# Kernel tuning notes

Hardware: AMD Instinct MI355X
Metric: run time of the kernel (lower is better)

Reference implementation:

```python
import jax, jax.numpy as jnp
import numpy as np

N = 2048      # num_nodes
B = 16        # batch
D_IN = 2      # input_dim per node
UNITS = 64    # rnn_units
F = D_IN + UNITS   # concat feature size = 66
M = 3         # num_matrices = (1 support + 1 adp hop)*K(=1) + 1 identity
E = N * 16    # sparse support edges (avg degree 16)


def _spmm(rows, cols, vals, x):
    # sparse support @ x, x: (N, K); equivalent of torch.sparse.mm
    return jax.ops.segment_sum(vals[:, None] * x[cols], rows, num_segments=N)


def _gconv(inputs, state, W, support_rows, support_cols, support_vals, adp):
    # inputs: (B, N*D_IN), state: (B, N*units) -> out: (B, N*out_dim)
    x = jnp.concatenate([inputs.reshape(B, N, -1), state.reshape(B, N, -1)], axis=2)  # (B,N,F)
    f = x.shape[2]
    x0 = x.transpose(1, 2, 0).reshape(N, f * B)                # (N, F*B)
    # diffusion step 1 over the single random_walk support
    x1 = _spmm(support_rows, support_cols, support_vals, x0)   # (N, F*B)
    # adaptive adjacency, k_hop=1 -> adp_lst = [adp], applied to x0
    x_temp = x0.reshape(N, f, B).transpose(2, 0, 1)            # (B,N,F)
    x2 = jnp.einsum('bnm,bmf->bnf', adp, x_temp)               # (B,N,F)
    x2 = x2.transpose(1, 2, 0).reshape(N, f * B)
    xs = jnp.stack([x0, x1, x2], axis=0)                       # (M,N,F*B)
    xs = xs.reshape(M, N, f, B).transpose(3, 1, 2, 0).reshape(B * N, f * M)
    out = xs @ W                                               # (B*N, out_dim)  (no bias: source never adds it)
    return out.reshape(B, N * W.shape[1])


def setup_inputs() -> dict:
    key = jax.random.key(0)
    ks = jax.random.split(key, 8)
    inputs = jax.random.normal(ks[0], (B, N * D_IN), dtype=jnp.float32)
    hx = jax.random.normal(ks[1], (B, N * UNITS), dtype=jnp.float32)
    adp = jax.random.uniform(ks[2], (B, N, N), dtype=jnp.float32) / N  # ~row-stochastic adaptive adj
    support_rows = jax.random.randint(ks[3], (E,), 0, N, dtype=jnp.int32)
    support_cols = jax.random.randint(ks[4], (E,), 0, N, dtype=jnp.int32)
    support_vals = jax.random.uniform(ks[5], (E,), dtype=jnp.float32) / 16.0
    W_ru = jax.random.normal(ks[6], (F * M, 2 * UNITS), dtype=jnp.float32) * 0.05
    W_c = jax.random.normal(ks[7], (F * M, UNITS), dtype=jnp.float32) * 0.05
    return dict(inputs=inputs, hx=hx, adp=adp, support_rows=support_rows,
                support_cols=support_cols, support_vals=support_vals,
                W_ru=W_ru, W_c=W_c, time_axis=0)


def reference(inputs, hx, adp, support_rows, support_cols, support_vals, W_ru, W_c, time_axis):
    # GRU with graph convolution gates (use_gc_for_ru=True, activation=tanh)
    ru = jax.nn.sigmoid(_gconv(inputs, hx, W_ru, support_rows, support_cols, support_vals, adp))
    ru = ru.reshape(B, N, 2 * UNITS)
    r = ru[..., :UNITS].reshape(B, N * UNITS)
    u = ru[..., UNITS:].reshape(B, N * UNITS)
    c = jnp.tanh(_gconv(inputs, r * hx, W_c, support_rows, support_cols, support_vals, adp))
    return u * hx + (1.0 - u) * c
```

## Files before the change

### kernel.cpp

```cpp
#include <hip/hip_runtime.h>
#include <cstdint>
#include <cstddef>

#define DN 2048
#define DB 16
#define DE 32768
#define FPAD 96

typedef __bf16 bf16x8 __attribute__((ext_vector_type(8)));
typedef float f32x4 __attribute__((ext_vector_type(4)));

__global__ __launch_bounds__(256) void prep_kernel(
    const float* __restrict__ inputs, const float* __restrict__ hx,
    const float* __restrict__ Wru, const float* __restrict__ Wc,
    __bf16* __restrict__ xcat1, __bf16* __restrict__ xcat2,
    __bf16* __restrict__ wtru, __bf16* __restrict__ wtc) {
  int idx = blockIdx.x * 256 + threadIdx.x;
  const int T1 = DB * DN * FPAD;
  if (idx < 2 * T1) {
    int which = idx >= T1 ? 1 : 0;
    int i = idx - which * T1;
    int f = i % FPAD;
    int bn = i / FPAD;
    int n = bn & (DN - 1);
    int b = bn >> 11;
    __bf16 v = (__bf16)0.0f;
    if (f < 2) v = (__bf16)inputs[(b << 12) + n * 2 + f];
    else if (f < 66 && !which) v = (__bf16)hx[((size_t)b << 17) + (n << 6) + (f - 2)];
    if (which) xcat2[i] = v; else xcat1[i] = v;
  } else {
    int j = idx - 2 * T1;
    if (j < 384 * FPAD) {
      int k = j % FPAD, o = j / FPAD;
      wtru[j] = (k < 66) ? (__bf16)Wru[(k * 3 + (o >> 7)) * 128 + (o & 127)] : (__bf16)0.0f;
    } else {
      j -= 384 * FPAD;
      if (j < 192 * FPAD) {
        int k = j % FPAD, o = j / FPAD;
        wtc[j] = (k < 66) ? (__bf16)Wc[(k * 3 + (o >> 6)) * 64 + (o & 63)] : (__bf16)0.0f;
      }
    }
  }
}

__global__ __launch_bounds__(1024) void build_csr(
    const int* __restrict__ rows, const int* __restrict__ cols,
    const float* __restrict__ vals,
    int* __restrict__ csr_ptr, int* __restrict__ csr_col,
    float* __restrict__ csr_val) {
  __shared__ int cnt[DN];
  __shared__ int sa[DN];
  __shared__ int sb[DN];
  int t = threadIdx.x;
  cnt[t] = 0; cnt[t + 1024] = 0;
  __syncthreads();
  for (int e = t; e < DE; e += 1024) atomicAdd(&cnt[rows[e]], 1);
  __syncthreads();
  sa[t] = cnt[t]; sa[t + 1024] = cnt[t + 1024];
  __syncthreads();
  int* src = sa; int* dst = sb;
  for (int off = 1; off < DN; off <<= 1) {
    for (int i = t; i < DN; i += 1024) {
      int v = src[i];
      if (i >= off) v += src[i - off];
      dst[i] = v;
    }
    __syncthreads();
    int* tmp = src; src = dst; dst = tmp;
  }
  int e0 = src[t] - cnt[t];
  int e1 = src[t + 1024] - cnt[t + 1024];
  csr_ptr[t] = e0; csr_ptr[t + 1024] = e1;
  if (t == 0) csr_ptr[DN] = DE;
  dst[t] = e0; dst[t + 1024] = e1;
  __syncthreads();
  for (int e = t; e < DE; e += 1024) {
    int r = rows[e];
    int p = atomicAdd(&dst[r], 1);
    csr_col[p] = cols[e];
    csr_val[p] = vals[e];
  }
}

template <int OD>
__global__ __launch_bounds__(256) void small_gemm(
    const __bf16* __restrict__ A, const __bf16* __restrict__ Bt,
    float* __restrict__ Y0, __bf16* __restrict__ y1b, __bf16* __restrict__ y2b) {
  __shared__ __attribute__((aligned(16))) __bf16 As[128 * 104];
  __shared__ __attribute__((aligned(16))) __bf16 Bs[64 * 104];
  int tid = threadIdx.x;
  int wave = tid >> 6, lane = tid & 63;
  int lrow = lane & 15, quad = lane >> 4;
  int r0 = blockIdx.x * 128;
  int c0 = blockIdx.y * 64;
  const uint4* gA = (const uint4*)(A + (size_t)r0 * FPAD);
  const uint4* gB = (const uint4*)(Bt + (size_t)c0 * FPAD);
  uint4* sA = (uint4*)As;
  uint4* sB = (uint4*)Bs;
#pragma unroll
  for (int i = 0; i < 6; ++i) {
    int s = i * 256 + tid;
    int r = s / 12, c4 = s % 12;
    sA[r * 13 + c4] = gA[r * 12 + c4];
  }
#pragma unroll
  for (int i = 0; i < 3; ++i) {
    int s = i * 256 + tid;
    int r = s / 12, c4 = s % 12;
    sB[r * 13 + c4] = gB[r * 12 + c4];
  }
  __syncthreads();
  int wm = wave >> 1, wn = wave & 1;
  f32x4 acc[4][2];
#pragma unroll
  for (int mt = 0; mt < 4; ++mt)
#pragma unroll
    for (int nt = 0; nt < 2; ++nt) acc[mt][nt] = (f32x4){0.f, 0.f, 0.f, 0.f};
#pragma unroll
  for (int kk = 0; kk < 3; ++kk) {
    bf16x8 af[4], bv[2];
#pragma unroll
    for (int mt = 0; mt < 4; ++mt)
      af[mt] = *(const bf16x8*)(As + (wm * 64 + mt * 16 + lrow) * 104 + kk * 32 + quad * 8);
#pragma unroll
    for (int nt = 0; nt < 2; ++nt)
      bv[nt] = *(const bf16x8*)(Bs + (wn * 32 + nt * 16 + lrow) * 104 + kk * 32 + quad * 8);
#pragma unroll
    for (int mt = 0; mt < 4; ++mt)
#pragma unroll
      for (int nt = 0; nt < 2; ++nt)
        acc[mt][nt] = __builtin_amdgcn_mfma_f32_16x16x32_bf16(af[mt], bv[nt], acc[mt][nt], 0, 0, 0);
  }
#pragma unroll
  for (int mt = 0; mt < 4; ++mt)
#pragma unroll
    for (int nt = 0; nt < 2; ++nt)
#pragma unroll
      for (int r = 0; r < 4; ++r) {
        int row = r0 + wm * 64 + mt * 16 + quad * 4 + r;
        int col = c0 + wn * 32 + nt * 16 + lrow;
        float v = acc[mt][nt][r];
        int g = col >> ((OD == 128) ? 7 : 6);
        int oo = col & (OD - 1);
        size_t oi = (size_t)row * OD + oo;
        if (g == 0) Y0[oi] = v;
        else if (g == 1) y1b[oi] = (__bf16)v;
        else y2b[oi] = (__bf16)v;
      }
}

template <int OD>
__global__ __launch_bounds__(256) void gather_pre(
    float* __restrict__ Y0, const __bf16* __restrict__ y1b,
    const int* __restrict__ csr_ptr, const int* __restrict__ csr_col,
    const float* __restrict__ csr_val) {
  constexpr int SH = (OD == 128) ? 7 : 6;
  int idx = blockIdx.x * 256 + threadIdx.x;
  int o = idx & (OD - 1);
  int bn = idx >> SH;
  int n = bn & (DN - 1);
  int b = bn >> 11;
  float acc = Y0[idx];
  int e1 = csr_ptr[n + 1];
  const __bf16* yb = y1b + ((size_t)b << 11) * OD;
  for (int e = csr_ptr[n]; e < e1; ++e)
    acc += csr_val[e] * (float)yb[(size_t)csr_col[e] * OD + o];
  Y0[idx] = acc;
}

template <int OD>
__global__ void transpose_y2(const __bf16* __restrict__ y2b, __bf16* __restrict__ y2t) {
  __shared__ __bf16 tile[32][33];
  int b = blockIdx.z;
  int mb = blockIdx.x * 32, ob = blockIdx.y * 32;
  int tx = threadIdx.x, ty = threadIdx.y;
#pragma unroll
  for (int i = 0; i < 4; ++i)
    tile[ty + i * 8][tx] = y2b[(size_t)(b * DN + mb + ty + i * 8) * OD + ob + tx];
  __syncthreads();
#pragma unroll
  for (int i = 0; i < 4; ++i)
    y2t[(size_t)(b * OD + ob + ty + i * 8) * DN + mb + tx] = tile[tx][ty + i * 8];
}

template <int OD, int WGM, int WGN, int MT, int NT, bool IS_RU>
__global__ __launch_bounds__(256) void adp_gemm(
    const float* __restrict__ adp, const __bf16* __restrict__ y2t,
    const float* __restrict__ pre, const float* __restrict__ hx,
    float* __restrict__ u_buf, __bf16* __restrict__ xcat2,
    float* __restrict__ outp) {
  constexpr int BM = WGM * MT * 16;
  constexpr int BN = WGN * NT * 16;
  constexpr int LDK = 72;
  constexpr int NA = (BM * 8) / 256;
  constexpr int NB = (BN * 8) / 256;
  __shared__ __attribute__((aligned(16))) __bf16 As[BM * LDK];
  __shared__ __attribute__((aligned(16))) __bf16 Bs[BN * LDK];
  int tid = threadIdx.x;
  int wave = tid >> 6, lane = tid & 63;
  int lrow = lane & 15, quad = lane >> 4;
  int b = blockIdx.y;
  int row0 = blockIdx.x * BM;
  const float* Ab = adp + ((size_t)b * DN + row0) * DN;
  const __bf16* Bb = y2t + (size_t)b * OD * DN;
  int wm = wave / WGN, wn = wave % WGN;
  f32x4 acc[MT][NT];
#pragma unroll
  for (int mt = 0; mt < MT; ++mt)
#pragma unroll
    for (int nt = 0; nt < NT; ++nt) acc[mt][nt] = (f32x4){0.f, 0.f, 0.f, 0.f};

  for (int c = 0; c < DN / 64; ++c) {
    int k0 = c * 64;
    f32x4 ra[NA][2];
    uint4 rb[NB];
#pragma unroll
    for (int i = 0; i < NA; ++i) {
      int s = i * 256 + tid, r = s >> 3, cc = s & 7;
      const float* p = Ab + (size_t)r * DN + k0 + cc * 8;
      ra[i][0] = *(const f32x4*)p;
      ra[i][1] = *(const f32x4*)(p + 4);
    }
#pragma unroll
    for (int i = 0; i < NB; ++i) {
      int s = i * 256 + tid, r = s >> 3, cc = s & 7;
      rb[i] = *(const uint4*)(Bb + (size_t)r * DN + k0 + cc * 8);
    }
    __syncthreads();
#pragma unroll
    for (int i = 0; i < NA; ++i) {
      int s = i * 256 + tid, r = s >> 3, cc = s & 7;
      bf16x8 cv;
#pragma unroll
      for (int j = 0; j < 4; ++j) cv[j] = (__bf16)ra[i][0][j];
#pragma unroll
      for (int j = 0; j < 4; ++j) cv[4 + j] = (__bf16)ra[i][1][j];
      *(bf16x8*)(As + r * LDK + cc * 8) = cv;
    }
#pragma unroll
    for (int i = 0; i < NB; ++i) {
      int s = i * 256 + tid, r = s >> 3, cc = s & 7;
      *(uint4*)(Bs + r * LDK + cc * 8) = rb[i];
    }
    __syncthreads();
#pragma unroll
    for (int kk = 0; kk < 2; ++kk) {
      bf16x8 af[MT], bv[NT];
#pragma unroll
      for (int mt = 0; mt < MT; ++mt) {
        int r = wm * MT * 16 + mt * 16 + lrow;
        af[mt] = *(const bf16x8*)(As + r * LDK + (kk * 4 + quad) * 8);
      }
#pragma unroll
      for (int nt = 0; nt < NT; ++nt) {
        int r = wn * NT * 16 + nt * 16 + lrow;
        bv[nt] = *(const bf16x8*)(Bs + r * LDK + (kk * 4 + quad) * 8);
      }
#pragma unroll
      for (int mt = 0; mt < MT; ++mt)
#pragma unroll
        for (int nt = 0; nt < NT; ++nt)
          acc[mt][nt] = __builtin_amdgcn_mfma_f32_16x16x32_bf16(af[mt], bv[nt], acc[mt][nt], 0, 0, 0);
    }
  }
#pragma unroll
  for (int mt = 0; mt < MT; ++mt)
#pragma unroll
    for (int nt = 0; nt < NT; ++nt)
#pragma unroll
      for (int r = 0; r < 4; ++r) {
        int n = row0 + wm * MT * 16 + mt * 16 + quad * 4 + r;
        int o = wn * NT * 16 + nt * 16 + lrow;
        float g = acc[mt][nt][r] + pre[((size_t)b * DN + n) * OD + o];
        if (IS_RU) {
          float s = 1.f / (1.f + __expf(-g));
          if (o < 64) {
            float hxv = hx[((size_t)b << 17) + n * 64 + o];
            xcat2[((size_t)b * DN + n) * FPAD + 2 + o] = (__bf16)(s * hxv);
          } else {
            u_buf[((size_t)b * DN + n) * 64 + (o - 64)] = s;
          }
        } else {
          float cval = 1.f - 2.f / (__expf(2.f * g) + 1.f);
          float u = u_buf[((size_t)b * DN + n) * 64 + o];
          float hxv = hx[((size_t)b << 17) + n * 64 + o];
          outp[((size_t)b << 17) + n * 64 + o] = u * hxv + (1.f - u) * cval;
        }
      }
}

extern "C" void kernel_launch(void* const* d_in, const int* in_sizes, int n_in,
                              void* d_out, int out_size, void* d_ws, size_t ws_size,
                              hipStream_t stream) {
  const float* inputs = (const float*)d_in[0];
  const float* hx     = (const float*)d_in[1];
  const float* adp    = (const float*)d_in[2];
  const int* srows    = (const int*)d_in[3];
  const int* scols    = (const int*)d_in[4];
  const float* svals  = (const float*)d_in[5];
  const float* Wru    = (const float*)d_in[6];
  const float* Wc     = (const float*)d_in[7];
  float* outp = (float*)d_out;

  char* w = (char*)d_ws;
  auto carve = [&](size_t bytes) -> char* {
    char* p = w;
    w += (bytes + 255) & ~(size_t)255;
    return p;
  };
  int*    csr_ptr = (int*)   carve((DN + 1) * sizeof(int));
  int*    csr_col = (int*)   carve(DE * sizeof(int));
  float*  csr_val = (float*) carve(DE * sizeof(float));
  __bf16* xcat1   = (__bf16*)carve((size_t)DB * DN * FPAD * 2);
  __bf16* xcat2   = (__bf16*)carve((size_t)DB * DN * FPAD * 2);
  __bf16* wtru    = (__bf16*)carve(384 * FPAD * 2);
  __bf16* wtc     = (__bf16*)carve(192 * FPAD * 2);
  float*  Y0      = (float*) carve((size_t)DB * DN * 128 * 4);
  __bf16* y1b     = (__bf16*)carve((size_t)DB * DN * 128 * 2);
  __bf16* y2b     = (__bf16*)carve((size_t)DB * DN * 128 * 2);
  __bf16* y2t     = (__bf16*)carve((size_t)DB * DN * 128 * 2);
  float*  u_buf   = (float*) carve((size_t)DB * DN * 64 * 4);
  (void)ws_size; (void)in_sizes; (void)n_in; (void)out_size;

  prep_kernel<<<24792, 256, 0, stream>>>(inputs, hx, Wru, Wc, xcat1, xcat2, wtru, wtc);
  build_csr<<<1, 1024, 0, stream>>>(srows, scols, svals, csr_ptr, csr_col, csr_val);

  small_gemm<128><<<dim3(256, 6), 256, 0, stream>>>(xcat1, wtru, Y0, y1b, y2b);
  gather_pre<128><<<16384, 256, 0, stream>>>(Y0, y1b, csr_ptr, csr_col, csr_val);
  transpose_y2<128><<<dim3(64, 4, 16), dim3(32, 8), 0, stream>>>(y2b, y2t);
  adp_gemm<128, 2, 2, 4, 4, true><<<dim3(16, 16), 256, 0, stream>>>(
      adp, y2t, Y0, hx, u_buf, xcat2, outp);

  small_gemm<64><<<dim3(256, 3), 256, 0, stream>>>(xcat2, wtc, Y0, y1b, y2b);
  gather_pre<64><<<8192, 256, 0, stream>>>(Y0, y1b, csr_ptr, csr_col, csr_val);
  transpose_y2<64><<<dim3(64, 2, 16), dim3(32, 8), 0, stream>>>(y2b, y2t);
  adp_gemm<64, 4, 1, 2, 4, false><<<dim3(16, 16), 256, 0, stream>>>(
      adp, y2t, Y0, hx, u_buf, xcat2, outp);
}
```

Baseline: 804.0 us.

## Prefetch adp tiles into registers, shrink adp GEMM row tile, parallelize CSR build

The adp GEMM now loads the next K-chunk of adp and y2t into registers while MFMAs run on the current shared-memory tile, overlapping global loads with compute. The row tile drops from 128 to 64, which doubles the grid to 512 blocks for better occupancy across CUs. The single-block CSR build is split into multi-block count, scan and scatter kernels, with the counter zeroed inside prep_kernel. This adds more kernel launches and more register pressure from the prefetch buffers, and the smaller row tile makes each block reload the full y2t operand.

```diff
diff --git a/kernel.cpp b/kernel.cpp
--- a/kernel.cpp
+++ b/kernel.cpp
@@ -14,7 +14,8 @@
     const float* __restrict__ inputs, const float* __restrict__ hx,
     const float* __restrict__ Wru, const float* __restrict__ Wc,
     __bf16* __restrict__ xcat1, __bf16* __restrict__ xcat2,
-    __bf16* __restrict__ wtru, __bf16* __restrict__ wtc) {
+    __bf16* __restrict__ wtru, __bf16* __restrict__ wtc,
+    int* __restrict__ cnt) {
   int idx = blockIdx.x * 256 + threadIdx.x;
   const int T1 = DB * DN * FPAD;
   if (idx < 2 * T1) {
@@ -38,48 +39,55 @@
       if (j < 192 * FPAD) {
         int k = j % FPAD, o = j / FPAD;
         wtc[j] = (k < 66) ? (__bf16)Wc[(k * 3 + (o >> 6)) * 64 + (o & 63)] : (__bf16)0.0f;
-      }
-    }
-  }
-}
-
-__global__ __launch_bounds__(1024) void build_csr(
-    const int* __restrict__ rows, const int* __restrict__ cols,
-    const float* __restrict__ vals,
-    int* __restrict__ csr_ptr, int* __restrict__ csr_col,
-    float* __restrict__ csr_val) {
-  __shared__ int cnt[DN];
+      } else {
+        j -= 192 * FPAD;
+        if (j < DN) cnt[j] = 0;
+      }
+    }
+  }
+}
+
+__global__ __launch_bounds__(512) void csr_count(const int* __restrict__ rows,
+                                                 int* __restrict__ cnt) {
+  int e = blockIdx.x * 512 + threadIdx.x;
+  atomicAdd(&cnt[rows[e]], 1);
+}
+
+__global__ __launch_bounds__(1024) void csr_scan(const int* __restrict__ cnt,
+                                                 int* __restrict__ csr_ptr,
+                                                 int* __restrict__ off) {
   __shared__ int sa[DN];
   __shared__ int sb[DN];
   int t = threadIdx.x;
-  cnt[t] = 0; cnt[t + 1024] = 0;
-  __syncthreads();
-  for (int e = t; e < DE; e += 1024) atomicAdd(&cnt[rows[e]], 1);
-  __syncthreads();
-  sa[t] = cnt[t]; sa[t + 1024] = cnt[t + 1024];
+  int c0 = cnt[t], c1 = cnt[t + 1024];
+  sa[t] = c0; sa[t + 1024] = c1;
   __syncthreads();
   int* src = sa; int* dst = sb;
-  for (int off = 1; off < DN; off <<= 1) {
+  for (int o = 1; o < DN; o <<= 1) {
     for (int i = t; i < DN; i += 1024) {
       int v = src[i];
-      if (i >= off) v += src[i - off];
+      if (i >= o) v += src[i - o];
       dst[i] = v;
     }
     __syncthreads();
     int* tmp = src; src = dst; dst = tmp;
   }
-  int e0 = src[t] - cnt[t];
-  int e1 = src[t + 1024] - cnt[t + 1024];
+  int e0 = src[t] - c0;
+  int e1 = src[t + 1024] - c1;
   csr_ptr[t] = e0; csr_ptr[t + 1024] = e1;
+  off[t] = e0; off[t + 1024] = e1;
   if (t == 0) csr_ptr[DN] = DE;
-  dst[t] = e0; dst[t + 1024] = e1;
-  __syncthreads();
-  for (int e = t; e < DE; e += 1024) {
-    int r = rows[e];
-    int p = atomicAdd(&dst[r], 1);
-    csr_col[p] = cols[e];
-    csr_val[p] = vals[e];
-  }
+}
+
+__global__ __launch_bounds__(512) void csr_scatter(
+    const int* __restrict__ rows, const int* __restrict__ cols,
+    const float* __restrict__ vals, int* __restrict__ off,
+    int* __restrict__ csr_col, float* __restrict__ csr_val) {
+  int e = blockIdx.x * 512 + threadIdx.x;
+  int r = rows[e];
+  int p = atomicAdd(&off[r], 1);
+  csr_col[p] = cols[e];
+  csr_val[p] = vals[e];
 }
 
 template <int OD>
@@ -183,14 +191,16 @@
     y2t[(size_t)(b * OD + ob + ty + i * 8) * DN + mb + tx] = tile[tx][ty + i * 8];
 }
 
-template <int OD, int WGM, int WGN, int MT, int NT, bool IS_RU>
+template <int OD, bool IS_RU>
 __global__ __launch_bounds__(256) void adp_gemm(
     const float* __restrict__ adp, const __bf16* __restrict__ y2t,
     const float* __restrict__ pre, const float* __restrict__ hx,
     float* __restrict__ u_buf, __bf16* __restrict__ xcat2,
     float* __restrict__ outp) {
-  constexpr int BM = WGM * MT * 16;
-  constexpr int BN = WGN * NT * 16;
+  constexpr int BM = 64;
+  constexpr int BN = OD;
+  constexpr int MT = 2;
+  constexpr int NT = OD / 32;
   constexpr int LDK = 72;
   constexpr int NA = (BM * 8) / 256;
   constexpr int NB = (BN * 8) / 256;
@@ -203,29 +213,29 @@
   int row0 = blockIdx.x * BM;
   const float* Ab = adp + ((size_t)b * DN + row0) * DN;
   const __bf16* Bb = y2t + (size_t)b * OD * DN;
-  int wm = wave / WGN, wn = wave % WGN;
+  int wm = wave >> 1, wn = wave & 1;
   f32x4 acc[MT][NT];
 #pragma unroll
   for (int mt = 0; mt < MT; ++mt)
 #pragma unroll
     for (int nt = 0; nt < NT; ++nt) acc[mt][nt] = (f32x4){0.f, 0.f, 0.f, 0.f};
 
+  f32x4 ra[NA][2];
+  uint4 rb[NB];
+#pragma unroll
+  for (int i = 0; i < NA; ++i) {
+    int s = i * 256 + tid, r = s >> 3, cc = s & 7;
+    const float* p = Ab + (size_t)r * DN + cc * 8;
+    ra[i][0] = *(const f32x4*)p;
+    ra[i][1] = *(const f32x4*)(p + 4);
+  }
+#pragma unroll
+  for (int i = 0; i < NB; ++i) {
+    int s = i * 256 + tid, r = s >> 3, cc = s & 7;
+    rb[i] = *(const uint4*)(Bb + (size_t)r * DN + cc * 8);
+  }
+
   for (int c = 0; c < DN / 64; ++c) {
-    int k0 = c * 64;
-    f32x4 ra[NA][2];
-    uint4 rb[NB];
-#pragma unroll
-    for (int i = 0; i < NA; ++i) {
-      int s = i * 256 + tid, r = s >> 3, cc = s & 7;
-      const float* p = Ab + (size_t)r * DN + k0 + cc * 8;
-      ra[i][0] = *(const f32x4*)p;
-      ra[i][1] = *(const f32x4*)(p + 4);
-    }
-#pragma unroll
-    for (int i = 0; i < NB; ++i) {
-      int s = i * 256 + tid, r = s >> 3, cc = s & 7;
-      rb[i] = *(const uint4*)(Bb + (size_t)r * DN + k0 + cc * 8);
-    }
     __syncthreads();
 #pragma unroll
     for (int i = 0; i < NA; ++i) {
@@ -243,17 +253,32 @@
       *(uint4*)(Bs + r * LDK + cc * 8) = rb[i];
     }
     __syncthreads();
+    if (c < DN / 64 - 1) {
+      int k0 = (c + 1) * 64;
+#pragma unroll
+      for (int i = 0; i < NA; ++i) {
+        int s = i * 256 + tid, r = s >> 3, cc = s & 7;
+        const float* p = Ab + (size_t)r * DN + k0 + cc * 8;
+        ra[i][0] = *(const f32x4*)p;
+        ra[i][1] = *(const f32x4*)(p + 4);
+      }
+#pragma unroll
+      for (int i = 0; i < NB; ++i) {
+        int s = i * 256 + tid, r = s >> 3, cc = s & 7;
+        rb[i] = *(const uint4*)(Bb + (size_t)r * DN + k0 + cc * 8);
+      }
+    }
 #pragma unroll
     for (int kk = 0; kk < 2; ++kk) {
       bf16x8 af[MT], bv[NT];
 #pragma unroll
       for (int mt = 0; mt < MT; ++mt) {
-        int r = wm * MT * 16 + mt * 16 + lrow;
+        int r = wm * 32 + mt * 16 + lrow;
         af[mt] = *(const bf16x8*)(As + r * LDK + (kk * 4 + quad) * 8);
       }
 #pragma unroll
       for (int nt = 0; nt < NT; ++nt) {
-        int r = wn * NT * 16 + nt * 16 + lrow;
+        int r = wn * (NT * 16) + nt * 16 + lrow;
         bv[nt] = *(const bf16x8*)(Bs + r * LDK + (kk * 4 + quad) * 8);
       }
 #pragma unroll
@@ -269,8 +294,8 @@
     for (int nt = 0; nt < NT; ++nt)
 #pragma unroll
       for (int r = 0; r < 4; ++r) {
-        int n = row0 + wm * MT * 16 + mt * 16 + quad * 4 + r;
-        int o = wn * NT * 16 + nt * 16 + lrow;
+        int n = row0 + wm * 32 + mt * 16 + quad * 4 + r;
+        int o = wn * (NT * 16) + nt * 16 + lrow;
         float g = acc[mt][nt][r] + pre[((size_t)b * DN + n) * OD + o];
         if (IS_RU) {
           float s = 1.f / (1.f + __expf(-g));
@@ -311,6 +336,8 @@
   int*    csr_ptr = (int*)   carve((DN + 1) * sizeof(int));
   int*    csr_col = (int*)   carve(DE * sizeof(int));
   float*  csr_val = (float*) carve(DE * sizeof(float));
+  int*    cnt     = (int*)   carve(DN * sizeof(int));
+  int*    off     = (int*)   carve(DN * sizeof(int));
   __bf16* xcat1   = (__bf16*)carve((size_t)DB * DN * FPAD * 2);
   __bf16* xcat2   = (__bf16*)carve((size_t)DB * DN * FPAD * 2);
   __bf16* wtru    = (__bf16*)carve(384 * FPAD * 2);
@@ -322,18 +349,21 @@
   float*  u_buf   = (float*) carve((size_t)DB * DN * 64 * 4);
   (void)ws_size; (void)in_sizes; (void)n_in; (void)out_size;
 
-  prep_kernel<<<24792, 256, 0, stream>>>(inputs, hx, Wru, Wc, xcat1, xcat2, wtru, wtc);
-  build_csr<<<1, 1024, 0, stream>>>(srows, scols, svals, csr_ptr, csr_col, csr_val);
+  prep_kernel<<<24800, 256, 0, stream>>>(inputs, hx, Wru, Wc, xcat1, xcat2,
+                                         wtru, wtc, cnt);
+  csr_count<<<64, 512, 0, stream>>>(srows, cnt);
+  csr_scan<<<1, 1024, 0, stream>>>(cnt, csr_ptr, off);
+  csr_scatter<<<64, 512, 0, stream>>>(srows, scols, svals, off, csr_col, csr_val);
 
   small_gemm<128><<<dim3(256, 6), 256, 0, stream>>>(xcat1, wtru, Y0, y1b, y2b);
   gather_pre<128><<<16384, 256, 0, stream>>>(Y0, y1b, csr_ptr, csr_col, csr_val);
   transpose_y2<128><<<dim3(64, 4, 16), dim3(32, 8), 0, stream>>>(y2b, y2t);
-  adp_gemm<128, 2, 2, 4, 4, true><<<dim3(16, 16), 256, 0, stream>>>(
+  adp_gemm<128, true><<<dim3(32, 16), 256, 0, stream>>>(
       adp, y2t, Y0, hx, u_buf, xcat2, outp);
 
   small_gemm<64><<<dim3(256, 3), 256, 0, stream>>>(xcat2, wtc, Y0, y1b, y2b);
   gather_pre<64><<<8192, 256, 0, stream>>>(Y0, y1b, csr_ptr, csr_col, csr_val);
   transpose_y2<64><<<dim3(64, 2, 16), dim3(32, 8), 0, stream>>>(y2b, y2t);
-  adp_gemm<64, 4, 1, 2, 4, false><<<dim3(16, 16), 256, 0, stream>>>(
+  adp_gemm<64, false><<<dim3(32, 16), 256, 0, stream>>>(
       adp, y2t, Y0, hx, u_buf, xcat2, outp);
 }
```

Result: faster. 721.8 us (-10.2%).
